# Kernel optimization log

Hardware: AMD Instinct MI355X
Metric: run time of the kernel (lower is better)

## Reference

```python
import jax, jax.numpy as jnp
import numpy as np

GRID_SIZE = 5
SPLINE_ORDER = 3
NUM_BASIS = GRID_SIZE + SPLINE_ORDER  # 8

def _grid():
    # Extended knot vector over [-1, 1]: G + 2k + 1 knots
    h = 2.0 / GRID_SIZE
    return jnp.asarray(-1.0 + h * np.arange(-SPLINE_ORDER, GRID_SIZE + SPLINE_ORDER + 1), dtype=jnp.float32)

def _bspline_basis(x, grid, k):
    # x: [B, D] -> bases [B, D, G + k] via Cox-de Boor recursion
    xe = x[..., None]
    b = ((xe >= grid[:-1]) & (xe < grid[1:])).astype(x.dtype)
    for p in range(1, k + 1):
        left = (xe - grid[:-(p + 1)]) / (grid[p:-1] - grid[:-(p + 1)]) * b[..., :-1]
        right = (grid[p + 1:] - xe) / (grid[p + 1:] - grid[1:-p]) * b[..., 1:]
        b = left + right
    return b

def setup_inputs() -> dict:
    key = jax.random.key(0)
    ks = jax.random.split(key, 10)
    B, D, U = 2048, 1024, 1024
    L = 3  # number of KAN sub-layers
    s = 0.05
    return {
        "x": jax.random.normal(ks[0], (B, D), jnp.float32),
        "h_prev": jax.random.normal(ks[1], (B, U), jnp.float32),
        "c_prev": jax.random.normal(ks[2], (B, U), jnp.float32),
        "lstm_kernel": jax.random.normal(ks[3], (D, 4 * U), jnp.float32) * s,
        "lstm_rkernel": jax.random.normal(ks[4], (U, 4 * U), jnp.float32) * s,
        "lstm_bias": jnp.zeros((4 * U,), jnp.float32),
        "kan_base_w": jax.random.normal(ks[5], (L, D, U), jnp.float32) * s,
        "kan_spline_w": jax.random.normal(ks[6], (L, D * NUM_BASIS, U), jnp.float32) * s,
        "combine_w": jax.random.normal(ks[7], (U + L * U, U), jnp.float32) * s,
        "combine_b": jnp.zeros((U,), jnp.float32),
    }

def reference(x, h_prev, c_prev, lstm_kernel, lstm_rkernel, lstm_bias,
              kan_base_w, kan_spline_w, combine_w, combine_b):
    B, D = x.shape
    L, _, U = kan_base_w.shape
    # --- LSTM cell (Keras gate order i, f, g, o) ---
    z = x @ lstm_kernel + h_prev @ lstm_rkernel + lstm_bias
    zi, zf, zg, zo = jnp.split(z, 4, axis=-1)
    c = jax.nn.sigmoid(zf) * c_prev + jax.nn.sigmoid(zi) * jnp.tanh(zg)
    h = jax.nn.sigmoid(zo) * jnp.tanh(c)
    lstm_out = h
    # --- KAN sub-layers: silu(x) @ W_base + Bspline(x) @ W_spline ---
    grid = _grid()
    bases = _bspline_basis(x, grid, SPLINE_ORDER)           # [B, D, K]
    base_out = jnp.einsum('bd,ldu->lbu', jax.nn.silu(x), kan_base_w)
    spline_w = kan_spline_w.reshape(L, D, NUM_BASIS, U)
    spline_out = jnp.einsum('bdk,ldku->lbu', bases, spline_w)
    kan_out = base_out + spline_out                          # [L, B, U]
    kan_concat = jnp.transpose(kan_out, (1, 0, 2)).reshape(B, L * U)
    # --- fuse ---
    combined = jnp.concatenate([lstm_out, kan_concat], axis=-1)
    output = combined @ combine_w + combine_b
    return (output, h, c)
```

## Files before the change

kernel.cpp:

```cpp
#include <hip/hip_runtime.h>
#include <hip/hip_bf16.h>
#include <math.h>

#define B_SZ 2048
#define D_SZ 1024
#define U_SZ 1024
#define L_SZ 3
#define NB 8
#define KAN_K (D_SZ + D_SZ * NB)
#define KAN_N (L_SZ * U_SZ)
#define LSTM_K (D_SZ + U_SZ)
#define COMB_K (U_SZ + L_SZ * U_SZ)
#define LSTM_N (4 * U_SZ)

typedef __attribute__((ext_vector_type(8))) short bhalf8_t;
typedef __attribute__((ext_vector_type(4))) float floatx4_t;

__device__ inline void async_copy16(const void* g, void* l) {
  __builtin_amdgcn_global_load_lds(
      (const __attribute__((address_space(1))) void*)g,
      (__attribute__((address_space(3))) void*)l, 16, 0, 0);
}

__global__ __launch_bounds__(256) void prep_trans(
    const float* __restrict__ x, const float* __restrict__ h_prev,
    const float* __restrict__ lstm_k, const float* __restrict__ lstm_r,
    const float* __restrict__ comb_w, const float* __restrict__ base_w,
    const float* __restrict__ spline_w,
    __hip_bfloat16* __restrict__ A1, __hip_bfloat16* __restrict__ Akan,
    __hip_bfloat16* __restrict__ Bt1, __hip_bfloat16* __restrict__ Btc,
    __hip_bfloat16* __restrict__ Btk) {
  __shared__ float tile[64][65];
  int bid = blockIdx.x;
  int tid = threadIdx.x;
  if (bid < 8192) {
    int idx = bid * 256 + tid;
    int b = idx >> 10, d = idx & 1023;
    float xv = x[idx];
    float hv = h_prev[idx];
    A1[(size_t)b * LSTM_K + d] = __float2bfloat16(xv);
    A1[(size_t)b * LSTM_K + D_SZ + d] = __float2bfloat16(hv);
    float sg = 1.0f / (1.0f + expf(-xv));
    Akan[(size_t)b * KAN_K + d] = __float2bfloat16(xv * sg);
    float t[12];
#pragma unroll
    for (int i = 0; i < 12; ++i) t[i] = (float)(-1.0 + 0.4 * (double)(i - 3));
    float bb[11];
#pragma unroll
    for (int j = 0; j < 11; ++j) bb[j] = (xv >= t[j] && xv < t[j + 1]) ? 1.0f : 0.0f;
#pragma unroll
    for (int p = 1; p <= 3; ++p) {
#pragma unroll
      for (int j = 0; j + p < 11; ++j) {
        float left = (xv - t[j]) / (t[j + p] - t[j]) * bb[j];
        float right = (t[j + p + 1] - xv) / (t[j + p + 1] - t[j + 1]) * bb[j + 1];
        bb[j] = left + right;
      }
    }
    __hip_bfloat16* dst = Akan + (size_t)b * KAN_K + D_SZ + d * 8;
#pragma unroll
    for (int j = 0; j < 8; ++j) dst[j] = __float2bfloat16(bb[j]);
    return;
  }
  int id = bid - 8192;
  const float* src;
  __hip_bfloat16* dst;
  int srcLd, dstLd, gxs;
  if (id < 1024) {
    src = lstm_k; dst = Bt1; srcLd = 4096; dstLd = 2048; gxs = 6;
  } else if (id < 2048) {
    id -= 1024; src = lstm_r; dst = Bt1 + 1024; srcLd = 4096; dstLd = 2048; gxs = 6;
  } else if (id < 3072) {
    id -= 2048; src = comb_w; dst = Btc; srcLd = 1024; dstLd = 4096; gxs = 4;
  } else if (id < 3840) {
    id -= 3072; int l = id >> 8; id &= 255;
    src = base_w + (size_t)l * 1048576;
    dst = Btk + (size_t)l * U_SZ * KAN_K;
    srcLd = 1024; dstLd = KAN_K; gxs = 4;
  } else {
    id -= 3840; int l = id >> 11; id &= 2047;
    src = spline_w + (size_t)l * 8388608;
    dst = Btk + (size_t)l * U_SZ * KAN_K + D_SZ;
    srcLd = 1024; dstLd = KAN_K; gxs = 4;
  }
  int n0 = (id & ((1 << gxs) - 1)) * 64;
  int k0 = (id >> gxs) * 64;
  int tx = tid & 63;
  int ty = tid >> 6;
#pragma unroll
  for (int i = 0; i < 16; ++i) {
    int r = ty + i * 4;
    tile[r][tx] = src[(size_t)(k0 + r) * srcLd + n0 + tx];
  }
  __syncthreads();
#pragma unroll
  for (int i = 0; i < 16; ++i) {
    int nq = ty + i * 4;
    dst[(size_t)(n0 + nq) * dstLd + k0 + tx] = __float2bfloat16(tile[tx][nq]);
  }
}

__device__ __forceinline__ void gemm_core(
    const __hip_bfloat16* __restrict__ A, const __hip_bfloat16* __restrict__ Bt,
    int lda, float* __restrict__ C, int ldc, int m0, int n0, int kBeg, int kEnd) {
  __shared__ __align__(16) char lds[32768];
  char* ldsA = lds;
  char* ldsB = lds + 16384;
  int tid = threadIdx.x;
  int lane = tid & 63;
  int wave = tid >> 6;
  int wm = wave >> 1, wn = wave & 1;
  int q = lane >> 4, l16 = lane & 15;

  floatx4_t acc[4][4];
#pragma unroll
  for (int i = 0; i < 4; ++i)
#pragma unroll
    for (int j = 0; j < 4; ++j) acc[i][j] = (floatx4_t){0.f, 0.f, 0.f, 0.f};

  const __hip_bfloat16* Ab = A + (size_t)m0 * lda;
  const __hip_bfloat16* Bb = Bt + (size_t)n0 * lda;

  for (int k0 = kBeg; k0 < kEnd; k0 += 64) {
#pragma unroll
    for (int it = 0; it < 4; ++it) {
      int L = tid + it * 256;
      int n = L >> 3;
      int c = (L & 7) ^ (n & 7);
      async_copy16((const char*)(Ab + (size_t)n * lda + k0) + c * 16, ldsA + L * 16);
    }
#pragma unroll
    for (int it = 0; it < 4; ++it) {
      int L = tid + it * 256;
      int n = L >> 3;
      int c = (L & 7) ^ (n & 7);
      async_copy16((const char*)(Bb + (size_t)n * lda + k0) + c * 16, ldsB + L * 16);
    }
    __syncthreads();
#pragma unroll
    for (int s = 0; s < 2; ++s) {
      bhalf8_t af[4], bf[4];
#pragma unroll
      for (int mt = 0; mt < 4; ++mt) {
        int row = wm * 64 + mt * 16 + l16;
        int p = (s * 4 + q) ^ (row & 7);
        af[mt] = *(const bhalf8_t*)(ldsA + row * 128 + p * 16);
      }
#pragma unroll
      for (int nt = 0; nt < 4; ++nt) {
        int row = wn * 64 + nt * 16 + l16;
        int p = (s * 4 + q) ^ (row & 7);
        bf[nt] = *(const bhalf8_t*)(ldsB + row * 128 + p * 16);
      }
#pragma unroll
      for (int mt = 0; mt < 4; ++mt)
#pragma unroll
        for (int nt = 0; nt < 4; ++nt)
          acc[mt][nt] = __builtin_amdgcn_mfma_f32_16x16x32_bf16(af[mt], bf[nt], acc[mt][nt], 0, 0, 0);
    }
    __syncthreads();
  }
#pragma unroll
  for (int mt = 0; mt < 4; ++mt) {
#pragma unroll
    for (int nt = 0; nt < 4; ++nt) {
      int ccol = n0 + wn * 64 + nt * 16 + l16;
#pragma unroll
      for (int i = 0; i < 4; ++i) {
        int crow = m0 + wm * 64 + mt * 16 + q * 4 + i;
        C[(size_t)crow * ldc + ccol] = acc[mt][nt][i];
      }
    }
  }
}

__global__ __launch_bounds__(256) void gemm_multi(
    const __hip_bfloat16* __restrict__ A1, const __hip_bfloat16* __restrict__ Bt1,
    const __hip_bfloat16* __restrict__ Akan, const __hip_bfloat16* __restrict__ Btk,
    float* __restrict__ z, float* __restrict__ Pkan) {
  int id = blockIdx.x;
  if (id < 512) {
    int n0 = (id & 31) * 128;
    int m0 = (id >> 5) * 128;
    gemm_core(A1, Bt1, LSTM_K, z, LSTM_N, m0, n0, 0, LSTM_K);
  } else {
    int id2 = id - 512;
    int sk = id2 >= 384;
    int rem = id2 - sk * 384;
    int n0 = (rem % 24) * 128;
    int m0 = (rem / 24) * 128;
    gemm_core(Akan, Btk, KAN_K, Pkan + (size_t)sk * B_SZ * KAN_N, KAN_N,
              m0, n0, sk * 4608, (sk + 1) * 4608);
  }
}

__global__ __launch_bounds__(256) void reduce_fuse(
    const float* __restrict__ z, const float* __restrict__ c_prev,
    const float* __restrict__ bias, const float* __restrict__ Pkan,
    float* __restrict__ h_out, float* __restrict__ c_out,
    __hip_bfloat16* __restrict__ Acomb) {
  int bid = blockIdx.x;
  int tid = threadIdx.x;
  if (bid < 8192) {
    int idx = bid * 256 + tid;
    int b = idx >> 10, u = idx & 1023;
    const float* zr = z + (size_t)b * LSTM_N;
    float zi = zr[u] + bias[u];
    float zf = zr[U_SZ + u] + bias[U_SZ + u];
    float zg = zr[2 * U_SZ + u] + bias[2 * U_SZ + u];
    float zo = zr[3 * U_SZ + u] + bias[3 * U_SZ + u];
    float si = 1.f / (1.f + expf(-zi));
    float sf = 1.f / (1.f + expf(-zf));
    float so = 1.f / (1.f + expf(-zo));
    float c = sf * c_prev[idx] + si * tanhf(zg);
    float h = so * tanhf(c);
    h_out[idx] = h;
    c_out[idx] = c;
    Acomb[(size_t)b * COMB_K + u] = __float2bfloat16(h);
  } else {
    int g = (bid - 8192) * 256 + tid;
    int m = g / (KAN_N / 4);
    int c4 = (g - m * (KAN_N / 4)) * 4;
    const float4 p0 = *(const float4*)(Pkan + (size_t)m * KAN_N + c4);
    const float4 p1 = *(const float4*)(Pkan + (size_t)B_SZ * KAN_N + (size_t)m * KAN_N + c4);
    __hip_bfloat16 o[4];
    o[0] = __float2bfloat16(p0.x + p1.x);
    o[1] = __float2bfloat16(p0.y + p1.y);
    o[2] = __float2bfloat16(p0.z + p1.z);
    o[3] = __float2bfloat16(p0.w + p1.w);
    *(ushort4*)(Acomb + (size_t)m * COMB_K + U_SZ + c4) = *(ushort4*)o;
  }
}

__global__ __launch_bounds__(256) void gemm_comb(
    const __hip_bfloat16* __restrict__ Acomb, const __hip_bfloat16* __restrict__ Btc,
    float* __restrict__ Pcomb) {
  int id = blockIdx.x;
  int sk = id >> 7;
  int rem = id & 127;
  int n0 = (rem & 7) * 128;
  int m0 = (rem >> 3) * 128;
  gemm_core(Acomb, Btc, COMB_K, Pcomb + (size_t)sk * B_SZ * U_SZ, U_SZ,
            m0, n0, sk * 1024, (sk + 1) * 1024);
}

__global__ __launch_bounds__(256) void comb_reduce(
    const float* __restrict__ Pcomb, const float* __restrict__ bias,
    float* __restrict__ out) {
  int g = blockIdx.x * 256 + threadIdx.x;
  int m = g >> 8;
  int c4 = (g & 255) * 4;
  float4 s = *(const float4*)(Pcomb + (size_t)m * U_SZ + c4);
  const size_t stride = (size_t)B_SZ * U_SZ;
#pragma unroll
  for (int p = 1; p < 4; ++p) {
    float4 t = *(const float4*)(Pcomb + stride * p + (size_t)m * U_SZ + c4);
    s.x += t.x; s.y += t.y; s.z += t.z; s.w += t.w;
  }
  float4 bv = *(const float4*)(bias + c4);
  s.x += bv.x; s.y += bv.y; s.z += bv.z; s.w += bv.w;
  *(float4*)(out + (size_t)m * U_SZ + c4) = s;
}

extern "C" void kernel_launch(void* const* d_in, const int* in_sizes, int n_in,
                              void* d_out, int out_size, void* d_ws, size_t ws_size,
                              hipStream_t stream) {
  const float* x        = (const float*)d_in[0];
  const float* h_prev   = (const float*)d_in[1];
  const float* c_prev   = (const float*)d_in[2];
  const float* lstm_k   = (const float*)d_in[3];
  const float* lstm_r   = (const float*)d_in[4];
  const float* lstm_b   = (const float*)d_in[5];
  const float* base_w   = (const float*)d_in[6];
  const float* spline_w = (const float*)d_in[7];
  const float* comb_w   = (const float*)d_in[8];
  const float* comb_b   = (const float*)d_in[9];
  float* out = (float*)d_out;

  char* ws = (char*)d_ws;
  auto alloc = [&](size_t bytes) {
    char* p = ws;
    ws += (bytes + 255) & ~(size_t)255;
    return p;
  };
  __hip_bfloat16* A1    = (__hip_bfloat16*)alloc((size_t)B_SZ * LSTM_K * 2);
  __hip_bfloat16* Akan  = (__hip_bfloat16*)alloc((size_t)B_SZ * KAN_K * 2);
  __hip_bfloat16* Acomb = (__hip_bfloat16*)alloc((size_t)B_SZ * COMB_K * 2);
  __hip_bfloat16* Bt1   = (__hip_bfloat16*)alloc((size_t)LSTM_N * LSTM_K * 2);
  __hip_bfloat16* Btk   = (__hip_bfloat16*)alloc((size_t)KAN_N * KAN_K * 2);
  __hip_bfloat16* Btc   = (__hip_bfloat16*)alloc((size_t)U_SZ * COMB_K * 2);
  float* z              = (float*)alloc((size_t)B_SZ * LSTM_N * 4);
  float* Pkan           = (float*)alloc((size_t)2 * B_SZ * KAN_N * 4);
  float* Pcomb          = Pkan;

  prep_trans<<<dim3(18176), 256, 0, stream>>>(x, h_prev, lstm_k, lstm_r, comb_w,
                                              base_w, spline_w, A1, Akan, Bt1, Btc, Btk);
  gemm_multi<<<dim3(1280), 256, 0, stream>>>(A1, Bt1, Akan, Btk, z, Pkan);
  reduce_fuse<<<dim3(14336), 256, 0, stream>>>(z, c_prev, lstm_b, Pkan,
                                               out + (size_t)B_SZ * U_SZ,
                                               out + 2 * (size_t)B_SZ * U_SZ, Acomb);
  gemm_comb<<<dim3(512), 256, 0, stream>>>(Acomb, Btc, Pcomb);
  comb_reduce<<<dim3(2048), 256, 0, stream>>>(Pcomb, comb_b, out);
}
```

Baseline: 577.4 us.

## Fuse all stages into one persistent cooperative kernel with grid syncs

New measurement: 876.9 us. 51.9% more time.

```diff
diff --git a/kernel.cpp b/kernel.cpp
--- a/kernel.cpp
+++ b/kernel.cpp
@@ -1,6 +1,9 @@
 #include <hip/hip_runtime.h>
+#include <hip/hip_cooperative_groups.h>
 #include <hip/hip_bf16.h>
 #include <math.h>
+
+namespace cg = cooperative_groups;
 
 #define B_SZ 2048
 #define D_SZ 1024
@@ -13,6 +16,12 @@
 #define COMB_K (U_SZ + L_SZ * U_SZ)
 #define LSTM_N (4 * U_SZ)
 
+#define P1_JOBS 18176
+#define P2_JOBS 1280
+#define P3_JOBS 14336
+#define P4_JOBS 512
+#define P5_JOBS 2048
+
 typedef __attribute__((ext_vector_type(8))) short bhalf8_t;
 typedef __attribute__((ext_vector_type(4))) float floatx4_t;
 
@@ -22,88 +31,17 @@
       (__attribute__((address_space(3))) void*)l, 16, 0, 0);
 }
 
-__global__ __launch_bounds__(256) void prep_trans(
-    const float* __restrict__ x, const float* __restrict__ h_prev,
-    const float* __restrict__ lstm_k, const float* __restrict__ lstm_r,
-    const float* __restrict__ comb_w, const float* __restrict__ base_w,
-    const float* __restrict__ spline_w,
-    __hip_bfloat16* __restrict__ A1, __hip_bfloat16* __restrict__ Akan,
-    __hip_bfloat16* __restrict__ Bt1, __hip_bfloat16* __restrict__ Btc,
-    __hip_bfloat16* __restrict__ Btk) {
-  __shared__ float tile[64][65];
-  int bid = blockIdx.x;
-  int tid = threadIdx.x;
-  if (bid < 8192) {
-    int idx = bid * 256 + tid;
-    int b = idx >> 10, d = idx & 1023;
-    float xv = x[idx];
-    float hv = h_prev[idx];
-    A1[(size_t)b * LSTM_K + d] = __float2bfloat16(xv);
-    A1[(size_t)b * LSTM_K + D_SZ + d] = __float2bfloat16(hv);
-    float sg = 1.0f / (1.0f + expf(-xv));
-    Akan[(size_t)b * KAN_K + d] = __float2bfloat16(xv * sg);
-    float t[12];
-#pragma unroll
-    for (int i = 0; i < 12; ++i) t[i] = (float)(-1.0 + 0.4 * (double)(i - 3));
-    float bb[11];
-#pragma unroll
-    for (int j = 0; j < 11; ++j) bb[j] = (xv >= t[j] && xv < t[j + 1]) ? 1.0f : 0.0f;
-#pragma unroll
-    for (int p = 1; p <= 3; ++p) {
-#pragma unroll
-      for (int j = 0; j + p < 11; ++j) {
-        float left = (xv - t[j]) / (t[j + p] - t[j]) * bb[j];
-        float right = (t[j + p + 1] - xv) / (t[j + p + 1] - t[j + 1]) * bb[j + 1];
-        bb[j] = left + right;
-      }
-    }
-    __hip_bfloat16* dst = Akan + (size_t)b * KAN_K + D_SZ + d * 8;
-#pragma unroll
-    for (int j = 0; j < 8; ++j) dst[j] = __float2bfloat16(bb[j]);
-    return;
-  }
-  int id = bid - 8192;
-  const float* src;
-  __hip_bfloat16* dst;
-  int srcLd, dstLd, gxs;
-  if (id < 1024) {
-    src = lstm_k; dst = Bt1; srcLd = 4096; dstLd = 2048; gxs = 6;
-  } else if (id < 2048) {
-    id -= 1024; src = lstm_r; dst = Bt1 + 1024; srcLd = 4096; dstLd = 2048; gxs = 6;
-  } else if (id < 3072) {
-    id -= 2048; src = comb_w; dst = Btc; srcLd = 1024; dstLd = 4096; gxs = 4;
-  } else if (id < 3840) {
-    id -= 3072; int l = id >> 8; id &= 255;
-    src = base_w + (size_t)l * 1048576;
-    dst = Btk + (size_t)l * U_SZ * KAN_K;
-    srcLd = 1024; dstLd = KAN_K; gxs = 4;
-  } else {
-    id -= 3840; int l = id >> 11; id &= 2047;
-    src = spline_w + (size_t)l * 8388608;
-    dst = Btk + (size_t)l * U_SZ * KAN_K + D_SZ;
-    srcLd = 1024; dstLd = KAN_K; gxs = 4;
-  }
-  int n0 = (id & ((1 << gxs) - 1)) * 64;
-  int k0 = (id >> gxs) * 64;
-  int tx = tid & 63;
-  int ty = tid >> 6;
-#pragma unroll
-  for (int i = 0; i < 16; ++i) {
-    int r = ty + i * 4;
-    tile[r][tx] = src[(size_t)(k0 + r) * srcLd + n0 + tx];
-  }
-  __syncthreads();
-#pragma unroll
-  for (int i = 0; i < 16; ++i) {
-    int nq = ty + i * 4;
-    dst[(size_t)(n0 + nq) * dstLd + k0 + tx] = __float2bfloat16(tile[tx][nq]);
-  }
+__device__ inline float fsig(float v) { return 1.f / (1.f + __expf(-v)); }
+__device__ inline float ftanh(float v) { return 1.f - 2.f / (__expf(2.f * v) + 1.f); }
+__device__ inline unsigned short bfb(float v) {
+  __hip_bfloat16 h = __float2bfloat16(v);
+  return *(unsigned short*)&h;
 }
 
 __device__ __forceinline__ void gemm_core(
     const __hip_bfloat16* __restrict__ A, const __hip_bfloat16* __restrict__ Bt,
-    int lda, float* __restrict__ C, int ldc, int m0, int n0, int kBeg, int kEnd) {
-  __shared__ __align__(16) char lds[32768];
+    int lda, float* __restrict__ C, int ldc, int m0, int n0, int kBeg, int kEnd,
+    char* lds) {
   char* ldsA = lds;
   char* ldsB = lds + 16384;
   int tid = threadIdx.x;
@@ -174,92 +112,177 @@
   }
 }
 
-__global__ __launch_bounds__(256) void gemm_multi(
-    const __hip_bfloat16* __restrict__ A1, const __hip_bfloat16* __restrict__ Bt1,
-    const __hip_bfloat16* __restrict__ Akan, const __hip_bfloat16* __restrict__ Btk,
-    float* __restrict__ z, float* __restrict__ Pkan) {
-  int id = blockIdx.x;
-  if (id < 512) {
-    int n0 = (id & 31) * 128;
-    int m0 = (id >> 5) * 128;
-    gemm_core(A1, Bt1, LSTM_K, z, LSTM_N, m0, n0, 0, LSTM_K);
-  } else {
-    int id2 = id - 512;
-    int sk = id2 >= 384;
-    int rem = id2 - sk * 384;
-    int n0 = (rem % 24) * 128;
-    int m0 = (rem / 24) * 128;
-    gemm_core(Akan, Btk, KAN_K, Pkan + (size_t)sk * B_SZ * KAN_N, KAN_N,
-              m0, n0, sk * 4608, (sk + 1) * 4608);
-  }
-}
-
-__global__ __launch_bounds__(256) void reduce_fuse(
-    const float* __restrict__ z, const float* __restrict__ c_prev,
-    const float* __restrict__ bias, const float* __restrict__ Pkan,
-    float* __restrict__ h_out, float* __restrict__ c_out,
-    __hip_bfloat16* __restrict__ Acomb) {
-  int bid = blockIdx.x;
+__global__ __launch_bounds__(256, 3) void fused_all(
+    const float* x, const float* h_prev, const float* c_prev,
+    const float* lstm_k, const float* lstm_r, const float* lstm_b,
+    const float* base_w, const float* spline_w, const float* comb_w,
+    const float* comb_b,
+    __hip_bfloat16* A1, __hip_bfloat16* Akan, __hip_bfloat16* Acomb,
+    __hip_bfloat16* Bt1, __hip_bfloat16* Btk, __hip_bfloat16* Btc,
+    float* z, float* Pkan, float* out, int* ctr) {
+  __shared__ __align__(16) char smem[32768];
+  __shared__ int jid;
+  cg::grid_group grid = cg::this_grid();
   int tid = threadIdx.x;
-  if (bid < 8192) {
-    int idx = bid * 256 + tid;
-    int b = idx >> 10, u = idx & 1023;
-    const float* zr = z + (size_t)b * LSTM_N;
-    float zi = zr[u] + bias[u];
-    float zf = zr[U_SZ + u] + bias[U_SZ + u];
-    float zg = zr[2 * U_SZ + u] + bias[2 * U_SZ + u];
-    float zo = zr[3 * U_SZ + u] + bias[3 * U_SZ + u];
-    float si = 1.f / (1.f + expf(-zi));
-    float sf = 1.f / (1.f + expf(-zf));
-    float so = 1.f / (1.f + expf(-zo));
-    float c = sf * c_prev[idx] + si * tanhf(zg);
-    float h = so * tanhf(c);
-    h_out[idx] = h;
-    c_out[idx] = c;
-    Acomb[(size_t)b * COMB_K + u] = __float2bfloat16(h);
-  } else {
-    int g = (bid - 8192) * 256 + tid;
-    int m = g / (KAN_N / 4);
-    int c4 = (g - m * (KAN_N / 4)) * 4;
-    const float4 p0 = *(const float4*)(Pkan + (size_t)m * KAN_N + c4);
-    const float4 p1 = *(const float4*)(Pkan + (size_t)B_SZ * KAN_N + (size_t)m * KAN_N + c4);
-    __hip_bfloat16 o[4];
-    o[0] = __float2bfloat16(p0.x + p1.x);
-    o[1] = __float2bfloat16(p0.y + p1.y);
-    o[2] = __float2bfloat16(p0.z + p1.z);
-    o[3] = __float2bfloat16(p0.w + p1.w);
-    *(ushort4*)(Acomb + (size_t)m * COMB_K + U_SZ + c4) = *(ushort4*)o;
-  }
-}
-
-__global__ __launch_bounds__(256) void gemm_comb(
-    const __hip_bfloat16* __restrict__ Acomb, const __hip_bfloat16* __restrict__ Btc,
-    float* __restrict__ Pcomb) {
-  int id = blockIdx.x;
-  int sk = id >> 7;
-  int rem = id & 127;
-  int n0 = (rem & 7) * 128;
-  int m0 = (rem >> 3) * 128;
-  gemm_core(Acomb, Btc, COMB_K, Pcomb + (size_t)sk * B_SZ * U_SZ, U_SZ,
-            m0, n0, sk * 1024, (sk + 1) * 1024);
-}
-
-__global__ __launch_bounds__(256) void comb_reduce(
-    const float* __restrict__ Pcomb, const float* __restrict__ bias,
-    float* __restrict__ out) {
-  int g = blockIdx.x * 256 + threadIdx.x;
-  int m = g >> 8;
-  int c4 = (g & 255) * 4;
-  float4 s = *(const float4*)(Pcomb + (size_t)m * U_SZ + c4);
-  const size_t stride = (size_t)B_SZ * U_SZ;
-#pragma unroll
-  for (int p = 1; p < 4; ++p) {
-    float4 t = *(const float4*)(Pcomb + stride * p + (size_t)m * U_SZ + c4);
-    s.x += t.x; s.y += t.y; s.z += t.z; s.w += t.w;
-  }
-  float4 bv = *(const float4*)(bias + c4);
-  s.x += bv.x; s.y += bv.y; s.z += bv.z; s.w += bv.w;
-  *(float4*)(out + (size_t)m * U_SZ + c4) = s;
+
+  if (blockIdx.x == 0 && tid == 0) *ctr = 0;
+  for (int job = blockIdx.x; job < P1_JOBS; job += gridDim.x) {
+    if (job < 8192) {
+      int idx = job * 256 + tid;
+      int b = idx >> 10, d = idx & 1023;
+      float xv = x[idx];
+      float hv = h_prev[idx];
+      A1[(size_t)b * LSTM_K + d] = __float2bfloat16(xv);
+      A1[(size_t)b * LSTM_K + D_SZ + d] = __float2bfloat16(hv);
+      float sg = 1.0f / (1.0f + __expf(-xv));
+      Akan[(size_t)b * KAN_K + d] = __float2bfloat16(xv * sg);
+      float t[12];
+#pragma unroll
+      for (int i = 0; i < 12; ++i) t[i] = (float)(-1.0 + 0.4 * (double)(i - 3));
+      float bb[11];
+#pragma unroll
+      for (int j = 0; j < 11; ++j) bb[j] = (xv >= t[j] && xv < t[j + 1]) ? 1.0f : 0.0f;
+#pragma unroll
+      for (int p = 1; p <= 3; ++p) {
+#pragma unroll
+        for (int j = 0; j + p < 11; ++j) {
+          float invl = 1.0f / (t[j + p] - t[j]);
+          float invr = 1.0f / (t[j + p + 1] - t[j + 1]);
+          bb[j] = (xv - t[j]) * invl * bb[j] + (t[j + p + 1] - xv) * invr * bb[j + 1];
+        }
+      }
+      unsigned short o[8];
+#pragma unroll
+      for (int j = 0; j < 8; ++j) o[j] = bfb(bb[j]);
+      *(uint4*)(Akan + (size_t)b * KAN_K + D_SZ + d * 8) = *(uint4*)o;
+    } else {
+      int id = job - 8192;
+      const float* src;
+      __hip_bfloat16* dst;
+      int srcLd, dstLd, gxs;
+      if (id < 1024) {
+        src = lstm_k; dst = Bt1; srcLd = 4096; dstLd = 2048; gxs = 6;
+      } else if (id < 2048) {
+        id -= 1024; src = lstm_r; dst = Bt1 + 1024; srcLd = 4096; dstLd = 2048; gxs = 6;
+      } else if (id < 3072) {
+        id -= 2048; src = comb_w; dst = Btc; srcLd = 1024; dstLd = 4096; gxs = 4;
+      } else if (id < 3840) {
+        id -= 3072; int l = id >> 8; id &= 255;
+        src = base_w + (size_t)l * 1048576;
+        dst = Btk + (size_t)l * U_SZ * KAN_K;
+        srcLd = 1024; dstLd = KAN_K; gxs = 4;
+      } else {
+        id -= 3840; int l = id >> 11; id &= 2047;
+        src = spline_w + (size_t)l * 8388608;
+        dst = Btk + (size_t)l * U_SZ * KAN_K + D_SZ;
+        srcLd = 1024; dstLd = KAN_K; gxs = 4;
+      }
+      int n0 = (id & ((1 << gxs) - 1)) * 64;
+      int k0 = (id >> gxs) * 64;
+      float (*tile)[65] = (float(*)[65])smem;
+      int tx = tid & 63;
+      int ty = tid >> 6;
+#pragma unroll
+      for (int i = 0; i < 16; ++i) {
+        int r = ty + i * 4;
+        tile[r][tx] = src[(size_t)(k0 + r) * srcLd + n0 + tx];
+      }
+      __syncthreads();
+      int kg = (tid & 15) * 4;
+      int nn = tid >> 4;
+#pragma unroll
+      for (int i = 0; i < 4; ++i) {
+        int n = nn + i * 16;
+        ushort4 w;
+        w.x = bfb(tile[kg + 0][n]);
+        w.y = bfb(tile[kg + 1][n]);
+        w.z = bfb(tile[kg + 2][n]);
+        w.w = bfb(tile[kg + 3][n]);
+        *(ushort4*)(dst + (size_t)(n0 + n) * dstLd + k0 + kg) = w;
+      }
+      __syncthreads();
+    }
+  }
+  grid.sync();
+
+  for (;;) {
+    if (tid == 0) jid = atomicAdd(ctr, 1);
+    __syncthreads();
+    int j = jid;
+    if (j >= P2_JOBS) break;
+    if (j < 768) {
+      int sk = j >= 384;
+      int rem = j - sk * 384;
+      int n0 = (rem % 24) * 128;
+      int m0 = (rem / 24) * 128;
+      gemm_core(Akan, Btk, KAN_K, Pkan + (size_t)sk * B_SZ * KAN_N, KAN_N,
+                m0, n0, sk * 4608, (sk + 1) * 4608, smem);
+    } else {
+      int j2 = j - 768;
+      int n0 = (j2 & 31) * 128;
+      int m0 = (j2 >> 5) * 128;
+      gemm_core(A1, Bt1, LSTM_K, z, LSTM_N, m0, n0, 0, LSTM_K, smem);
+    }
+  }
+  grid.sync();
+
+  float* h_out = out + (size_t)B_SZ * U_SZ;
+  float* c_out = out + 2 * (size_t)B_SZ * U_SZ;
+  for (int job = blockIdx.x; job < P3_JOBS; job += gridDim.x) {
+    if (job < 8192) {
+      int idx = job * 256 + tid;
+      int b = idx >> 10, u = idx & 1023;
+      const float* zr = z + (size_t)b * LSTM_N;
+      float zi = zr[u] + lstm_b[u];
+      float zf = zr[U_SZ + u] + lstm_b[U_SZ + u];
+      float zg = zr[2 * U_SZ + u] + lstm_b[2 * U_SZ + u];
+      float zo = zr[3 * U_SZ + u] + lstm_b[3 * U_SZ + u];
+      float c = fsig(zf) * c_prev[idx] + fsig(zi) * ftanh(zg);
+      float h = fsig(zo) * ftanh(c);
+      h_out[idx] = h;
+      c_out[idx] = c;
+      Acomb[(size_t)b * COMB_K + u] = __float2bfloat16(h);
+    } else {
+      int g = (job - 8192) * 256 + tid;
+      int m = g / (KAN_N / 4);
+      int c4 = (g - m * (KAN_N / 4)) * 4;
+      const float4 p0 = *(const float4*)(Pkan + (size_t)m * KAN_N + c4);
+      const float4 p1 = *(const float4*)(Pkan + (size_t)B_SZ * KAN_N + (size_t)m * KAN_N + c4);
+      ushort4 o;
+      o.x = bfb(p0.x + p1.x);
+      o.y = bfb(p0.y + p1.y);
+      o.z = bfb(p0.z + p1.z);
+      o.w = bfb(p0.w + p1.w);
+      *(ushort4*)(Acomb + (size_t)m * COMB_K + U_SZ + c4) = o;
+    }
+  }
+  grid.sync();
+
+  for (int j = blockIdx.x; j < P4_JOBS; j += gridDim.x) {
+    int sk = j >> 7;
+    int rem = j & 127;
+    int n0 = (rem & 7) * 128;
+    int m0 = (rem >> 3) * 128;
+    gemm_core(Acomb, Btc, COMB_K, Pkan + (size_t)sk * B_SZ * U_SZ, U_SZ,
+              m0, n0, sk * 1024, (sk + 1) * 1024, smem);
+  }
+  grid.sync();
+
+  for (int g0 = blockIdx.x; g0 < P5_JOBS; g0 += gridDim.x) {
+    int g = g0 * 256 + tid;
+    int m = g >> 8;
+    int c4 = (g & 255) * 4;
+    float4 s = *(const float4*)(Pkan + (size_t)m * U_SZ + c4);
+    const size_t stride = (size_t)B_SZ * U_SZ;
+#pragma unroll
+    for (int p = 1; p < 4; ++p) {
+      float4 t = *(const float4*)(Pkan + stride * p + (size_t)m * U_SZ + c4);
+      s.x += t.x; s.y += t.y; s.z += t.z; s.w += t.w;
+    }
+    float4 bv = *(const float4*)(comb_b + c4);
+    s.x += bv.x; s.y += bv.y; s.z += bv.z; s.w += bv.w;
+    *(float4*)(out + (size_t)m * U_SZ + c4) = s;
+  }
 }
 
 extern "C" void kernel_launch(void* const* d_in, const int* in_sizes, int n_in,
@@ -291,14 +314,19 @@
   __hip_bfloat16* Btc   = (__hip_bfloat16*)alloc((size_t)U_SZ * COMB_K * 2);
   float* z              = (float*)alloc((size_t)B_SZ * LSTM_N * 4);
   float* Pkan           = (float*)alloc((size_t)2 * B_SZ * KAN_N * 4);
-  float* Pcomb          = Pkan;
-
-  prep_trans<<<dim3(18176), 256, 0, stream>>>(x, h_prev, lstm_k, lstm_r, comb_w,
-                                              base_w, spline_w, A1, Akan, Bt1, Btc, Btk);
-  gemm_multi<<<dim3(1280), 256, 0, stream>>>(A1, Bt1, Akan, Btk, z, Pkan);
-  reduce_fuse<<<dim3(14336), 256, 0, stream>>>(z, c_prev, lstm_b, Pkan,
-                                               out + (size_t)B_SZ * U_SZ,
-                                               out + 2 * (size_t)B_SZ * U_SZ, Acomb);
-  gemm_comb<<<dim3(512), 256, 0, stream>>>(Acomb, Btc, Pcomb);
-  comb_reduce<<<dim3(2048), 256, 0, stream>>>(Pcomb, comb_b, out);
-}
+  int* ctr              = (int*)alloc(256);
+
+  int nb = 0;
+  if (hipOccupancyMaxActiveBlocksPerMultiprocessor(&nb, (const void*)fused_all, 256, 0) != hipSuccess || nb < 1)
+    nb = 2;
+  int gridBlocks = nb * 256;
+  if (gridBlocks > 768) gridBlocks = 768;
+
+  void* args[] = {
+      (void*)&x, (void*)&h_prev, (void*)&c_prev, (void*)&lstm_k, (void*)&lstm_r,
+      (void*)&lstm_b, (void*)&base_w, (void*)&spline_w, (void*)&comb_w, (void*)&comb_b,
+      (void*)&A1, (void*)&Akan, (void*)&Acomb, (void*)&Bt1, (void*)&Btk, (void*)&Btc,
+      (void*)&z, (void*)&Pkan, (void*)&out, (void*)&ctr};
+  hipLaunchCooperativeKernel((const void*)fused_all, dim3(gridBlocks), dim3(256),
+                             args, 0, stream);
+}
```

## Vectorize prep transposes and stores, use fast math, reorder GEMM block dispatch

Applied to the files above, without the earlier changes.

After: 510.1 us. 1.13x faster.

```diff
diff --git a/kernel.cpp b/kernel.cpp
--- a/kernel.cpp
+++ b/kernel.cpp
@@ -20,6 +20,13 @@
   __builtin_amdgcn_global_load_lds(
       (const __attribute__((address_space(1))) void*)g,
       (__attribute__((address_space(3))) void*)l, 16, 0, 0);
+}
+
+__device__ inline float fsig(float v) { return 1.f / (1.f + __expf(-v)); }
+__device__ inline float ftanh(float v) { return 1.f - 2.f / (__expf(2.f * v) + 1.f); }
+__device__ inline unsigned short bfb(float v) {
+  __hip_bfloat16 h = __float2bfloat16(v);
+  return *(unsigned short*)&h;
 }
 
 __global__ __launch_bounds__(256) void prep_trans(
@@ -40,7 +47,7 @@
     float hv = h_prev[idx];
     A1[(size_t)b * LSTM_K + d] = __float2bfloat16(xv);
     A1[(size_t)b * LSTM_K + D_SZ + d] = __float2bfloat16(hv);
-    float sg = 1.0f / (1.0f + expf(-xv));
+    float sg = 1.0f / (1.0f + __expf(-xv));
     Akan[(size_t)b * KAN_K + d] = __float2bfloat16(xv * sg);
     float t[12];
 #pragma unroll
@@ -52,14 +59,15 @@
     for (int p = 1; p <= 3; ++p) {
 #pragma unroll
       for (int j = 0; j + p < 11; ++j) {
-        float left = (xv - t[j]) / (t[j + p] - t[j]) * bb[j];
-        float right = (t[j + p + 1] - xv) / (t[j + p + 1] - t[j + 1]) * bb[j + 1];
-        bb[j] = left + right;
+        float invl = 1.0f / (t[j + p] - t[j]);
+        float invr = 1.0f / (t[j + p + 1] - t[j + 1]);
+        bb[j] = (xv - t[j]) * invl * bb[j] + (t[j + p + 1] - xv) * invr * bb[j + 1];
       }
     }
-    __hip_bfloat16* dst = Akan + (size_t)b * KAN_K + D_SZ + d * 8;
-#pragma unroll
-    for (int j = 0; j < 8; ++j) dst[j] = __float2bfloat16(bb[j]);
+    unsigned short o[8];
+#pragma unroll
+    for (int j = 0; j < 8; ++j) o[j] = bfb(bb[j]);
+    *(uint4*)(Akan + (size_t)b * KAN_K + D_SZ + d * 8) = *(uint4*)o;
     return;
   }
   int id = bid - 8192;
@@ -85,18 +93,29 @@
   }
   int n0 = (id & ((1 << gxs) - 1)) * 64;
   int k0 = (id >> gxs) * 64;
-  int tx = tid & 63;
-  int ty = tid >> 6;
-#pragma unroll
-  for (int i = 0; i < 16; ++i) {
-    int r = ty + i * 4;
-    tile[r][tx] = src[(size_t)(k0 + r) * srcLd + n0 + tx];
+  int c4 = (tid & 15) * 4;
+  int r0 = tid >> 4;
+#pragma unroll
+  for (int i = 0; i < 4; ++i) {
+    int r = r0 + i * 16;
+    const float4 v = *(const float4*)(src + (size_t)(k0 + r) * srcLd + n0 + c4);
+    tile[r][c4 + 0] = v.x;
+    tile[r][c4 + 1] = v.y;
+    tile[r][c4 + 2] = v.z;
+    tile[r][c4 + 3] = v.w;
   }
   __syncthreads();
-#pragma unroll
-  for (int i = 0; i < 16; ++i) {
-    int nq = ty + i * 4;
-    dst[(size_t)(n0 + nq) * dstLd + k0 + tx] = __float2bfloat16(tile[tx][nq]);
+  int kg = (tid & 15) * 4;
+  int nn = tid >> 4;
+#pragma unroll
+  for (int i = 0; i < 4; ++i) {
+    int n = nn + i * 16;
+    ushort4 w;
+    w.x = bfb(tile[kg + 0][n]);
+    w.y = bfb(tile[kg + 1][n]);
+    w.z = bfb(tile[kg + 2][n]);
+    w.w = bfb(tile[kg + 3][n]);
+    *(ushort4*)(dst + (size_t)(n0 + n) * dstLd + k0 + kg) = w;
   }
 }
 
@@ -179,18 +198,18 @@
     const __hip_bfloat16* __restrict__ Akan, const __hip_bfloat16* __restrict__ Btk,
     float* __restrict__ z, float* __restrict__ Pkan) {
   int id = blockIdx.x;
-  if (id < 512) {
-    int n0 = (id & 31) * 128;
-    int m0 = (id >> 5) * 128;
-    gemm_core(A1, Bt1, LSTM_K, z, LSTM_N, m0, n0, 0, LSTM_K);
-  } else {
-    int id2 = id - 512;
-    int sk = id2 >= 384;
-    int rem = id2 - sk * 384;
+  if (id < 768) {
+    int sk = id >= 384;
+    int rem = id - sk * 384;
     int n0 = (rem % 24) * 128;
     int m0 = (rem / 24) * 128;
     gemm_core(Akan, Btk, KAN_K, Pkan + (size_t)sk * B_SZ * KAN_N, KAN_N,
               m0, n0, sk * 4608, (sk + 1) * 4608);
+  } else {
+    int j2 = id - 768;
+    int n0 = (j2 & 31) * 128;
+    int m0 = (j2 >> 5) * 128;
+    gemm_core(A1, Bt1, LSTM_K, z, LSTM_N, m0, n0, 0, LSTM_K);
   }
 }
 
@@ -209,11 +228,8 @@
     float zf = zr[U_SZ + u] + bias[U_SZ + u];
     float zg = zr[2 * U_SZ + u] + bias[2 * U_SZ + u];
     float zo = zr[3 * U_SZ + u] + bias[3 * U_SZ + u];
-    float si = 1.f / (1.f + expf(-zi));
-    float sf = 1.f / (1.f + expf(-zf));
-    float so = 1.f / (1.f + expf(-zo));
-    float c = sf * c_prev[idx] + si * tanhf(zg);
-    float h = so * tanhf(c);
+    float c = fsig(zf) * c_prev[idx] + fsig(zi) * ftanh(zg);
+    float h = fsig(zo) * ftanh(c);
     h_out[idx] = h;
     c_out[idx] = c;
     Acomb[(size_t)b * COMB_K + u] = __float2bfloat16(h);
@@ -223,12 +239,12 @@
     int c4 = (g - m * (KAN_N / 4)) * 4;
     const float4 p0 = *(const float4*)(Pkan + (size_t)m * KAN_N + c4);
     const float4 p1 = *(const float4*)(Pkan + (size_t)B_SZ * KAN_N + (size_t)m * KAN_N + c4);
-    __hip_bfloat16 o[4];
-    o[0] = __float2bfloat16(p0.x + p1.x);
-    o[1] = __float2bfloat16(p0.y + p1.y);
-    o[2] = __float2bfloat16(p0.z + p1.z);
-    o[3] = __float2bfloat16(p0.w + p1.w);
-    *(ushort4*)(Acomb + (size_t)m * COMB_K + U_SZ + c4) = *(ushort4*)o;
+    ushort4 o;
+    o.x = bfb(p0.x + p1.x);
+    o.y = bfb(p0.y + p1.y);
+    o.z = bfb(p0.z + p1.z);
+    o.w = bfb(p0.w + p1.w);
+    *(ushort4*)(Acomb + (size_t)m * COMB_K + U_SZ + c4) = o;
   }
 }
 
```
